# Kernel tuning notes

Measured on AMD Instinct MI355X. Metric: run time of the kernel, lower is better.

## Reference

```python
import jax, jax.numpy as jnp
import numpy as np

N, M, D, S = 4, 256, 32, 32


def setup_inputs() -> dict:
    key = jax.random.key(0)
    k1, k2 = jax.random.split(key)
    inputs = jax.random.normal(k1, (N, M, M, D), dtype=jnp.float32)
    mask = jnp.ones((N, M, 1), dtype=bool)
    coeffs = jax.random.normal(k2, (D, S, 15), dtype=jnp.float32) * np.sqrt(2.0) / (D + S)
    diag_bias = jnp.zeros((1, S, 1, 1), dtype=jnp.float32)
    all_bias = jnp.zeros((1, S, 1, 1), dtype=jnp.float32)
    return {"inputs": inputs, "mask": mask, "coeffs": coeffs,
            "diag_bias": diag_bias, "all_bias": all_bias}


def _contractions_2_to_2(x):
    # x: [N, D, m, m]; returns list of 15 [N, D, m, m] basis tensors ('inf' normalization)
    n, d, m, _ = x.shape
    diag = jnp.diagonal(x, axis1=2, axis2=3)            # [N, D, m]
    sum_diag = jnp.sum(diag, axis=2, keepdims=True)      # [N, D, 1]
    rows = jnp.sum(x, axis=3)                            # [N, D, m]
    cols = jnp.sum(x, axis=2)                            # [N, D, m]
    tot = jnp.sum(rows, axis=2)                          # [N, D]
    eye = jnp.eye(m, dtype=x.dtype)

    def diag_embed(v):  # v: [N, D, m] -> [N, D, m, m]
        return v[..., :, None] * eye

    full = x.shape
    op1 = diag_embed(diag)
    op2 = diag_embed(jnp.broadcast_to(sum_diag, diag.shape)) / m
    op3 = diag_embed(rows) / m
    op4 = diag_embed(cols) / m
    op5 = diag_embed(jnp.broadcast_to(tot[..., None], diag.shape)) / (m ** 2)
    op6 = jnp.broadcast_to(cols[..., :, None], full) / m
    op7 = jnp.broadcast_to(rows[..., :, None], full) / m
    op8 = jnp.broadcast_to(cols[..., None, :], full) / m
    op9 = jnp.broadcast_to(rows[..., None, :], full) / m
    op10 = x
    op11 = jnp.swapaxes(x, 2, 3)
    op12 = jnp.broadcast_to(diag[..., :, None], full)
    op13 = jnp.broadcast_to(diag[..., None, :], full)
    op14 = jnp.broadcast_to(sum_diag[..., None], full) / m
    op15 = jnp.broadcast_to(tot[..., None, None], full) / (m ** 2)
    return [op1, op2, op3, op4, op5, op6, op7, op8, op9, op10,
            op11, op12, op13, op14, op15]


def reference(inputs, mask, coeffs, diag_bias, all_bias):
    # inputs: [N, m, m, D] -> [N, D, m, m]
    x = jnp.transpose(inputs, (0, 3, 1, 2))
    m = x.shape[3]
    ops = _contractions_2_to_2(x)
    # einsum('dsb,ndbij->nsij') expressed as accumulation over the 15 bases
    # (avoids materializing the [N, D, 15, m, m] stack)
    out = jnp.zeros((x.shape[0], coeffs.shape[1], m, m), dtype=x.dtype)
    for b, op in enumerate(ops):
        out = out + jnp.einsum('ds,ndij->nsij', coeffs[:, :, b], op)
    eye = jnp.eye(m, dtype=x.dtype)[None, None]
    out = out + all_bias + eye * diag_bias
    return jnp.transpose(out, (0, 2, 3, 1))  # [N, m, m, S]
```

## Files before the change

kernel.cpp:

```cpp
#include <hip/hip_runtime.h>


#define NN 4
#define MM 256
#define DD 32
#define SS 32

#define WS_ROWS   0
#define WS_COLSA  32768
#define WS_COLSB  65536
#define WS_DIAG   98304
#define WS_RW     131072
#define WS_CW     163840
#define WS_DW     196608
#define WS_SD     229376
#define WS_TOT    229504
#define WS_CPACK  229632

__global__ __launch_bounds__(256) void k_reduce(const float* __restrict__ in,
                                                const float* __restrict__ coeffs,
                                                float* __restrict__ ws) {
    int blk = blockIdx.x;
    int t = threadIdx.x;
    if (blk < 256) {
        int n = blk >> 6;
        int rem = blk & 63;
        int half = rem >> 5;
        int jt = rem & 31;
        int j = jt * 8 + (t >> 5);
        int d = t & 31;
        const float* base = in + ((size_t)n * MM * MM + j) * DD + d
                               + (size_t)half * 128 * MM * DD;
        float acc = 0.f;
        #pragma unroll 8
        for (int i = 0; i < 128; ++i) acc += base[(size_t)i * MM * DD];
        float* dst = ws + (half ? WS_COLSB : WS_COLSA);
        dst[(n * MM + j) * DD + d] = acc;
    } else if (blk < 256 + NN * MM) {
        int nm = blk - 256;
        int n = nm >> 8;
        int ii = nm & 255;
        int d = t & 31, g = t >> 5;
        const float* base = in + (size_t)nm * MM * DD + d;
        float acc = 0.f;
        for (int j = g; j < MM; j += 8) acc += base[(size_t)j * DD];
        __shared__ float red[256];
        red[t] = acc;
        __syncthreads();
        if (t < 32) {
            float s = 0.f;
            #pragma unroll
            for (int g2 = 0; g2 < 8; ++g2) s += red[g2 * 32 + t];
            ws[WS_ROWS + nm * DD + t] = s;
            float dv = in[((size_t)nm * MM + ii) * DD + t];
            ws[WS_DIAG + nm * DD + t] = dv;
            atomicAdd(ws + WS_TOT + n * DD + t, s);
            atomicAdd(ws + WS_SD + n * DD + t, dv);
        }
    } else {
        for (int idx = t; idx < 15 * DD * SS; idx += 256) {
            int plane = idx >> 10;
            int ds = idx & 1023;
            ws[WS_CPACK + plane * (DD * SS) + ds] = coeffs[ds * 15 + plane];
        }
    }
}

__global__ __launch_bounds__(256) void k_aux(const float* __restrict__ diag_bias,
                                             const float* __restrict__ all_bias,
                                             float* __restrict__ ws) {
    int idx = blockIdx.x * blockDim.x + threadIdx.x;
    int s = idx & 31;
    int nm = idx >> 5;
    int n = nm >> 8;
    const float inv_m = 1.0f / MM;
    const float inv_m2 = inv_m * inv_m;
    float u = 0.f, v = 0.f, dgacc = 0.f, w = 0.f;
    for (int d = 0; d < DD; ++d) {
        const float* cp = ws + WS_CPACK + d * SS + s;
        float r = ws[WS_ROWS + nm * DD + d];
        float cl = ws[WS_COLSA + nm * DD + d] + ws[WS_COLSB + nm * DD + d];
        float dv = ws[WS_DIAG + nm * DD + d];
        float sdv = ws[WS_SD + n * DD + d];
        float totv = ws[WS_TOT + n * DD + d];
        u += cp[5 * 1024] * cl * inv_m + cp[6 * 1024] * r * inv_m + cp[11 * 1024] * dv;
        v += cp[7 * 1024] * cl * inv_m + cp[8 * 1024] * r * inv_m + cp[12 * 1024] * dv;
        dgacc += cp[0] * dv + cp[1 * 1024] * sdv * inv_m + cp[2 * 1024] * r * inv_m
               + cp[3 * 1024] * cl * inv_m + cp[4 * 1024] * totv * inv_m2;
        w += cp[13 * 1024] * sdv * inv_m + cp[14 * 1024] * totv * inv_m2;
    }
    ws[WS_RW + idx] = u + w + all_bias[s];
    ws[WS_CW + idx] = v;
    ws[WS_DW + idx] = dgacc + diag_bias[s];
}

__global__ __launch_bounds__(256, 2) void k_main(const float* __restrict__ in,
                                                 const float* __restrict__ ws,
                                                 float* __restrict__ out) {
    int b = blockIdx.x;
    int tjb = b & 15;
    int tib = (b >> 4) & 15;
    int n = b >> 8;
    int tj = threadIdx.x & 15, ti = threadIdx.x >> 4;
    int i = tib * 16 + ti, j = tjb * 16 + tj;

    const float4* A = (const float4*)(in + (((size_t)(n * MM + i)) * MM + j) * DD);
    const float4* B = (const float4*)(in + (((size_t)(n * MM + j)) * MM + i) * DD);

    float4 av[8], bv[8];
    #pragma unroll
    for (int q = 0; q < 8; ++q) av[q] = A[q];
    #pragma unroll
    for (int q = 0; q < 8; ++q) bv[q] = B[q];

    const float4* rw = (const float4*)(ws + WS_RW + (n * MM + i) * SS);
    const float4* cw = (const float4*)(ws + WS_CW + (n * MM + j) * SS);
    float acc[SS];
    #pragma unroll
    for (int q = 0; q < 8; ++q) {
        float4 x = rw[q], y = cw[q];
        acc[q * 4 + 0] = x.x + y.x;
        acc[q * 4 + 1] = x.y + y.y;
        acc[q * 4 + 2] = x.z + y.z;
        acc[q * 4 + 3] = x.w + y.w;
    }
    if (i == j) {
        const float4* dw = (const float4*)(ws + WS_DW + (n * MM + i) * SS);
        #pragma unroll
        for (int q = 0; q < 8; ++q) {
            float4 dq = dw[q];
            acc[q * 4 + 0] += dq.x;
            acc[q * 4 + 1] += dq.y;
            acc[q * 4 + 2] += dq.z;
            acc[q * 4 + 3] += dq.w;
        }
    }

    const float* c10 = ws + WS_CPACK + 9 * (DD * SS);
    const float* c11 = ws + WS_CPACK + 10 * (DD * SS);
    #pragma unroll
    for (int dq = 0; dq < 8; ++dq) {
        const float* ca = c10 + dq * 4 * SS;
        const float* cb = c11 + dq * 4 * SS;
        #pragma unroll
        for (int r = 0; r < 4; ++r) {
            float a = (r == 0) ? av[dq].x : (r == 1) ? av[dq].y : (r == 2) ? av[dq].z : av[dq].w;
            float bb = (r == 0) ? bv[dq].x : (r == 1) ? bv[dq].y : (r == 2) ? bv[dq].z : bv[dq].w;
            #pragma unroll
            for (int s = 0; s < SS; ++s) {
                acc[s] = fmaf(a, ca[r * SS + s], acc[s]);
                acc[s] = fmaf(bb, cb[r * SS + s], acc[s]);
            }
        }
    }

    float4* o = (float4*)(out + (((size_t)(n * MM + i)) * MM + j) * SS);
    #pragma unroll
    for (int q = 0; q < 8; ++q)
        o[q] = make_float4(acc[q * 4 + 0], acc[q * 4 + 1], acc[q * 4 + 2], acc[q * 4 + 3]);
}

extern "C" void kernel_launch(void* const* d_in, const int* in_sizes, int n_in,
                              void* d_out, int out_size, void* d_ws, size_t ws_size,
                              hipStream_t stream) {
    const float* in = (const float*)d_in[0];
    const float* coeffs = (const float*)d_in[2];
    const float* diag_bias = (const float*)d_in[3];
    const float* all_bias = (const float*)d_in[4];
    float* out = (float*)d_out;
    float* ws = (float*)d_ws;

    hipMemsetAsync((char*)d_ws + (size_t)WS_SD * 4, 0, 256 * sizeof(float), stream);
    k_reduce<<<256 + NN * MM + 1, 256, 0, stream>>>(in, coeffs, ws);
    k_aux<<<(NN * MM * SS) / 256, 256, 0, stream>>>(diag_bias, all_bias, ws);
    k_main<<<NN * 16 * 16, 256, 0, stream>>>(in, ws, out);
}
```

Before: 146.7 us.

## Vectorize reduction loads with float4 and reorder main-kernel loads

```diff
diff --git a/kernel.cpp b/kernel.cpp
--- a/kernel.cpp
+++ b/kernel.cpp
@@ -7,55 +7,68 @@
 #define SS 32
 
 #define WS_ROWS   0
-#define WS_COLSA  32768
-#define WS_COLSB  65536
-#define WS_DIAG   98304
-#define WS_RW     131072
-#define WS_CW     163840
-#define WS_DW     196608
-#define WS_SD     229376
-#define WS_TOT    229504
-#define WS_CPACK  229632
+#define WS_DIAG   32768
+#define WS_COLSP  65536
+#define WS_RW     196608
+#define WS_CW     229376
+#define WS_DW     262144
+#define WS_SD     294912
+#define WS_TOT    295040
+#define WS_CPACK  295168
 
 __global__ __launch_bounds__(256) void k_reduce(const float* __restrict__ in,
                                                 const float* __restrict__ coeffs,
                                                 float* __restrict__ ws) {
     int blk = blockIdx.x;
     int t = threadIdx.x;
-    if (blk < 256) {
-        int n = blk >> 6;
-        int rem = blk & 63;
-        int half = rem >> 5;
-        int jt = rem & 31;
-        int j = jt * 8 + (t >> 5);
-        int d = t & 31;
-        const float* base = in + ((size_t)n * MM * MM + j) * DD + d
-                               + (size_t)half * 128 * MM * DD;
-        float acc = 0.f;
+    if (blk < 128) {
+        int n = blk >> 5;
+        int rem = blk & 31;
+        int jb = rem >> 2, ih = rem & 3;
+        int i0 = ih * 64, j0 = jb * 32;
+        int jl = t >> 3, d4 = t & 7;
+        const float4* base = (const float4*)in;
+        size_t idx0 = ((size_t)(n * MM + i0) * MM + (j0 + jl)) * 8 + d4;
+        float4 a = {0.f, 0.f, 0.f, 0.f};
         #pragma unroll 8
-        for (int i = 0; i < 128; ++i) acc += base[(size_t)i * MM * DD];
-        float* dst = ws + (half ? WS_COLSB : WS_COLSA);
-        dst[(n * MM + j) * DD + d] = acc;
-    } else if (blk < 256 + NN * MM) {
-        int nm = blk - 256;
+        for (int i = 0; i < 64; ++i) {
+            float4 v = base[idx0 + (size_t)i * MM * 8];
+            a.x += v.x; a.y += v.y; a.z += v.z; a.w += v.w;
+        }
+        ((float4*)(ws + WS_COLSP))[(size_t)ih * 8192 + (n * MM + j0 + jl) * 8 + d4] = a;
+    } else if (blk < 128 + NN * MM) {
+        int nm = blk - 128;
         int n = nm >> 8;
         int ii = nm & 255;
-        int d = t & 31, g = t >> 5;
-        const float* base = in + (size_t)nm * MM * DD + d;
-        float acc = 0.f;
-        for (int j = g; j < MM; j += 8) acc += base[(size_t)j * DD];
-        __shared__ float red[256];
-        red[t] = acc;
+        int d4 = t & 7, jg = t >> 3;
+        const float4* base = (const float4*)(in + (size_t)nm * MM * DD);
+        float4 a = {0.f, 0.f, 0.f, 0.f};
+        #pragma unroll
+        for (int k = 0; k < 8; ++k) {
+            float4 v = base[(jg * 8 + k) * 8 + d4];
+            a.x += v.x; a.y += v.y; a.z += v.z; a.w += v.w;
+        }
+        __shared__ float4 red[256];
+        red[t] = a;
         __syncthreads();
-        if (t < 32) {
-            float s = 0.f;
-            #pragma unroll
-            for (int g2 = 0; g2 < 8; ++g2) s += red[g2 * 32 + t];
-            ws[WS_ROWS + nm * DD + t] = s;
-            float dv = in[((size_t)nm * MM + ii) * DD + t];
-            ws[WS_DIAG + nm * DD + t] = dv;
-            atomicAdd(ws + WS_TOT + n * DD + t, s);
-            atomicAdd(ws + WS_SD + n * DD + t, dv);
+        if (t < 8) {
+            float4 s = {0.f, 0.f, 0.f, 0.f};
+            #pragma unroll 8
+            for (int g = 0; g < 32; ++g) {
+                float4 v = red[g * 8 + t];
+                s.x += v.x; s.y += v.y; s.z += v.z; s.w += v.w;
+            }
+            ((float4*)(ws + WS_ROWS))[nm * 8 + t] = s;
+            float4 dv = ((const float4*)in)[((size_t)nm * MM + ii) * 8 + t];
+            ((float4*)(ws + WS_DIAG))[nm * 8 + t] = dv;
+            atomicAdd(ws + WS_TOT + n * DD + t * 4 + 0, s.x);
+            atomicAdd(ws + WS_TOT + n * DD + t * 4 + 1, s.y);
+            atomicAdd(ws + WS_TOT + n * DD + t * 4 + 2, s.z);
+            atomicAdd(ws + WS_TOT + n * DD + t * 4 + 3, s.w);
+            atomicAdd(ws + WS_SD + n * DD + t * 4 + 0, dv.x);
+            atomicAdd(ws + WS_SD + n * DD + t * 4 + 1, dv.y);
+            atomicAdd(ws + WS_SD + n * DD + t * 4 + 2, dv.z);
+            atomicAdd(ws + WS_SD + n * DD + t * 4 + 3, dv.w);
         }
     } else {
         for (int idx = t; idx < 15 * DD * SS; idx += 256) {
@@ -79,7 +92,10 @@
     for (int d = 0; d < DD; ++d) {
         const float* cp = ws + WS_CPACK + d * SS + s;
         float r = ws[WS_ROWS + nm * DD + d];
-        float cl = ws[WS_COLSA + nm * DD + d] + ws[WS_COLSB + nm * DD + d];
+        float cl = ws[WS_COLSP + 0 * 32768 + nm * DD + d]
+                 + ws[WS_COLSP + 1 * 32768 + nm * DD + d]
+                 + ws[WS_COLSP + 2 * 32768 + nm * DD + d]
+                 + ws[WS_COLSP + 3 * 32768 + nm * DD + d];
         float dv = ws[WS_DIAG + nm * DD + d];
         float sdv = ws[WS_SD + n * DD + d];
         float totv = ws[WS_TOT + n * DD + d];
@@ -94,9 +110,9 @@
     ws[WS_DW + idx] = dgacc + diag_bias[s];
 }
 
-__global__ __launch_bounds__(256, 2) void k_main(const float* __restrict__ in,
-                                                 const float* __restrict__ ws,
-                                                 float* __restrict__ out) {
+__global__ __launch_bounds__(256) void k_main(const float* __restrict__ in,
+                                              const float* __restrict__ ws,
+                                              float* __restrict__ out) {
     int b = blockIdx.x;
     int tjb = b & 15;
     int tib = (b >> 4) & 15;
@@ -104,25 +120,22 @@
     int tj = threadIdx.x & 15, ti = threadIdx.x >> 4;
     int i = tib * 16 + ti, j = tjb * 16 + tj;
 
-    const float4* A = (const float4*)(in + (((size_t)(n * MM + i)) * MM + j) * DD);
-    const float4* B = (const float4*)(in + (((size_t)(n * MM + j)) * MM + i) * DD);
-
-    float4 av[8], bv[8];
-    #pragma unroll
-    for (int q = 0; q < 8; ++q) av[q] = A[q];
-    #pragma unroll
-    for (int q = 0; q < 8; ++q) bv[q] = B[q];
-
     const float4* rw = (const float4*)(ws + WS_RW + (n * MM + i) * SS);
     const float4* cw = (const float4*)(ws + WS_CW + (n * MM + j) * SS);
+    float4 rv[8], cv[8];
+    #pragma unroll
+    for (int q = 0; q < 8; ++q) rv[q] = rw[q];
+    #pragma unroll
+    for (int q = 0; q < 8; ++q) cv[q] = cw[q];
+    __builtin_amdgcn_sched_barrier(0);
+
     float acc[SS];
     #pragma unroll
     for (int q = 0; q < 8; ++q) {
-        float4 x = rw[q], y = cw[q];
-        acc[q * 4 + 0] = x.x + y.x;
-        acc[q * 4 + 1] = x.y + y.y;
-        acc[q * 4 + 2] = x.z + y.z;
-        acc[q * 4 + 3] = x.w + y.w;
+        acc[q * 4 + 0] = rv[q].x + cv[q].x;
+        acc[q * 4 + 1] = rv[q].y + cv[q].y;
+        acc[q * 4 + 2] = rv[q].z + cv[q].z;
+        acc[q * 4 + 3] = rv[q].w + cv[q].w;
     }
     if (i == j) {
         const float4* dw = (const float4*)(ws + WS_DW + (n * MM + i) * SS);
@@ -135,6 +148,15 @@
             acc[q * 4 + 3] += dq.w;
         }
     }
+
+    const float4* A = (const float4*)(in + (((size_t)(n * MM + i)) * MM + j) * DD);
+    const float4* B = (const float4*)(in + (((size_t)(n * MM + j)) * MM + i) * DD);
+    float4 av[8], bv[8];
+    #pragma unroll
+    for (int q = 0; q < 8; ++q) av[q] = A[q];
+    #pragma unroll
+    for (int q = 0; q < 8; ++q) bv[q] = B[q];
+    __builtin_amdgcn_sched_barrier(0);
 
     const float* c10 = ws + WS_CPACK + 9 * (DD * SS);
     const float* c11 = ws + WS_CPACK + 10 * (DD * SS);
@@ -171,7 +193,7 @@
     float* ws = (float*)d_ws;
 
     hipMemsetAsync((char*)d_ws + (size_t)WS_SD * 4, 0, 256 * sizeof(float), stream);
-    k_reduce<<<256 + NN * MM + 1, 256, 0, stream>>>(in, coeffs, ws);
+    k_reduce<<<128 + NN * MM + 1, 256, 0, stream>>>(in, coeffs, ws);
     k_aux<<<(NN * MM * SS) / 256, 256, 0, stream>>>(diag_bias, all_bias, ws);
     k_main<<<NN * 16 * 16, 256, 0, stream>>>(in, ws, out);
 }
```

New measurement: 164.0 us. +11.8%, slower.
